# Optimization experiments

Hardware: AMD Instinct MI355X
Metric: run time of the kernel (lower is better)

Reference implementation:

```python
import jax, jax.numpy as jnp
import numpy as np

NEG_INF = -1e38

def wkv(w, u, k, v):
    """Numerically-stable RWKV-4 WKV recurrence.
    w, u: [C] (log-space decay / first-token bonus)
    k, v: [B, T, C]
    returns y: [B, T, C]
    """
    B, T, C = k.shape

    def step(carry, kv):
        p, q, o = carry          # numerator state, denominator state, running log-max; each [B, C]
        kt, vt = kv              # [B, C]
        # output at t (includes the u-boosted current token)
        no = jnp.maximum(o, u + kt)
        A = jnp.exp(o - no)
        Bt = jnp.exp(u + kt - no)
        y = (A * p + Bt * vt) / (A * q + Bt)
        # state update (decay by w, absorb current token)
        no2 = jnp.maximum(w + o, kt)
        A2 = jnp.exp(w + o - no2)
        B2 = jnp.exp(kt - no2)
        return (A2 * p + B2 * vt, A2 * q + B2, no2), y

    init = (jnp.zeros((B, C), k.dtype), jnp.zeros((B, C), k.dtype),
            jnp.full((B, C), NEG_INF, k.dtype))
    kT = jnp.swapaxes(k, 0, 1)   # [T, B, C]
    vT = jnp.swapaxes(v, 0, 1)
    _, ys = jax.lax.scan(step, init, (kT, vT))
    return jnp.swapaxes(ys, 0, 1)


def setup_inputs() -> dict:
    key = jax.random.key(0)
    ks = jax.random.split(key, 10)
    B, T, C = 8, 4096, 512
    scale = 1.0 / np.sqrt(C)
    return {
        "x": jax.random.normal(ks[0], (B, T, C), jnp.float32),
        "spatial_decay": jax.random.normal(ks[1], (C,), jnp.float32),
        "spatial_first": jax.random.normal(ks[2], (C,), jnp.float32),
        "mix_k": jax.random.uniform(ks[3], (1, 1, C), jnp.float32),
        "mix_v": jax.random.uniform(ks[4], (1, 1, C), jnp.float32),
        "mix_r": jax.random.uniform(ks[5], (1, 1, C), jnp.float32),
        "wk": jax.random.normal(ks[6], (C, C), jnp.float32) * scale,
        "wv": jax.random.normal(ks[7], (C, C), jnp.float32) * scale,
        "wr": jax.random.normal(ks[8], (C, C), jnp.float32) * scale,
        "wo": jax.random.normal(ks[9], (C, C), jnp.float32) * scale,
    }


def reference(x, spatial_decay, spatial_first, mix_k, mix_v, mix_r, wk, wv, wr, wo):
    B, T, C = x.shape
    # time_shift: xx[t] = x[t-1], xx[0] = 0  (ZeroPad2d((0,0,1,-1)))
    xx = jnp.pad(x, ((0, 0), (1, 0), (0, 0)))[:, :-1]
    xk = x * mix_k + xx * (1.0 - mix_k)
    xv = x * mix_v + xx * (1.0 - mix_v)
    xr = x * mix_r + xx * (1.0 - mix_r)
    k = jnp.einsum('btc,cd->btd', xk, wk)
    v = jnp.einsum('btc,cd->btd', xv, wv)
    r = jnp.einsum('btc,cd->btd', xr, wr)
    sr = jax.nn.sigmoid(r)
    y = wkv(spatial_decay / T, spatial_first / T, k, v)
    return jnp.einsum('btc,cd->btd', sr * y, wo)
```

## Files before the change

### kernel.cpp

```cpp
#include <hip/hip_runtime.h>

#define BB 8
#define TT 4096
#define CC 512
#define MM (BB * TT)
#define SS 128
#define LL 32

typedef short short8 __attribute__((ext_vector_type(8)));
typedef unsigned short ushort8 __attribute__((ext_vector_type(8)));
typedef float f32x4 __attribute__((ext_vector_type(4)));

__device__ __forceinline__ unsigned short f2bf(float f) {
    unsigned int u = __float_as_uint(f);
    u += 0x7FFFu + ((u >> 16) & 1u);
    return (unsigned short)(u >> 16);
}
__device__ __forceinline__ float bf2f(unsigned short h) {
    return __uint_as_float(((unsigned int)h) << 16);
}

__device__ __forceinline__ void gl_lds16(const void* g, void* l) {
    __builtin_amdgcn_global_load_lds(
        (__attribute__((address_space(1))) void*)(unsigned long long)g,
        (__attribute__((address_space(3))) void*)(unsigned int)(unsigned long long)l,
        16, 0, 0);
}

__device__ __forceinline__ ushort8 pack8(f32x4 a, f32x4 b) {
    ushort8 r;
    r[0] = f2bf(a.x); r[1] = f2bf(a.y); r[2] = f2bf(a.z); r[3] = f2bf(a.w);
    r[4] = f2bf(b.x); r[5] = f2bf(b.y); r[6] = f2bf(b.z); r[7] = f2bf(b.w);
    return r;
}

__global__ __launch_bounds__(256) void prep(
    const float* __restrict__ x,
    const float* __restrict__ mixk, const float* __restrict__ mixv,
    const float* __restrict__ mixr,
    const float* __restrict__ wk, const float* __restrict__ wv,
    const float* __restrict__ wr, const float* __restrict__ wo,
    unsigned short* __restrict__ wT,
    unsigned short* __restrict__ kx, unsigned short* __restrict__ vx,
    unsigned short* __restrict__ rx) {
    __shared__ float t[64][65];
    if (blockIdx.x < 256) {
        const int bid = blockIdx.x;
        const int which = bid >> 6;
        const int rem = bid & 63;
        const int k0 = (rem >> 3) * 64;
        const int n0 = (rem & 7) * 64;
        const float* src = (which == 0) ? wk : (which == 1) ? wv
                         : (which == 2) ? wr : wo;
        const int r = threadIdx.x >> 6;
        const int c = threadIdx.x & 63;
#pragma unroll
        for (int p = 0; p < 16; ++p)
            t[p * 4 + r][c] = src[(size_t)(k0 + p * 4 + r) * CC + n0 + c];
        __syncthreads();
        unsigned short* dst = wT + (size_t)which * (CC * CC);
#pragma unroll
        for (int p = 0; p < 16; ++p)
            dst[(size_t)(n0 + p * 4 + r) * CC + k0 + c] = f2bf(t[c][p * 4 + r]);
        return;
    }
    const int idx = (blockIdx.x - 256) * 256 + threadIdx.x;
    const int row = idx >> 6;
    const int ch  = (idx & 63) * 8;
    const int tt  = row & (TT - 1);
    const size_t off = (size_t)row * CC + ch;
    const float* xr = x + off;

    const f32x4 zero4 = {0.f, 0.f, 0.f, 0.f};
    const f32x4 one4  = {1.f, 1.f, 1.f, 1.f};

    f32x4 xc0 = ((const f32x4*)xr)[0];
    f32x4 xc1 = ((const f32x4*)xr)[1];
    f32x4 xp0 = zero4, xp1 = zero4;
    if (tt != 0) {
        xp0 = ((const f32x4*)(xr - CC))[0];
        xp1 = ((const f32x4*)(xr - CC))[1];
    }

    f32x4 m0, m1;
    m0 = ((const f32x4*)(mixk + ch))[0];
    m1 = ((const f32x4*)(mixk + ch))[1];
    *(ushort8*)(kx + off) = pack8(xc0 * m0 + xp0 * (one4 - m0),
                                  xc1 * m1 + xp1 * (one4 - m1));
    m0 = ((const f32x4*)(mixv + ch))[0];
    m1 = ((const f32x4*)(mixv + ch))[1];
    *(ushort8*)(vx + off) = pack8(xc0 * m0 + xp0 * (one4 - m0),
                                  xc1 * m1 + xp1 * (one4 - m1));
    m0 = ((const f32x4*)(mixr + ch))[0];
    m1 = ((const f32x4*)(mixr + ch))[1];
    *(ushort8*)(rx + off) = pack8(xc0 * m0 + xp0 * (one4 - m0),
                                  xc1 * m1 + xp1 * (one4 - m1));
}

template <bool F32OUT>
__device__ __forceinline__ void gemm_body(
    const unsigned short* __restrict__ A,
    const unsigned short* __restrict__ Bw,
    void* __restrict__ OutP, const int sig,
    const int pm, const int pn) {
    __shared__ unsigned short As[3][128 * 32];
    __shared__ unsigned short Bs[3][256 * 32];

    const int tid = threadIdx.x;
    const int ar = tid >> 2;
    const int cg = (tid & 3) ^ ((tid >> 3) & 3);
    const unsigned short* agA = A  + (size_t)(pm * 128 + ar) * CC + cg * 8;
    const unsigned short* agB = Bw + (size_t)(pn * 256 + ar) * CC + cg * 8;

    const int w = tid >> 6, lane = tid & 63;
    const int wr = w >> 1, wc = w & 1;
    const int q = lane >> 4, l16 = lane & 15;
    const int sw = (q ^ ((l16 >> 1) & 3)) * 8;

    f32x4 acc[4][8];
#pragma unroll
    for (int i = 0; i < 4; i++)
#pragma unroll
        for (int j = 0; j < 8; j++) acc[i][j] = (f32x4){0.f, 0.f, 0.f, 0.f};

#define STG(bi, k0) do {                                                        \
    gl_lds16(agA + (k0), &As[bi][tid * 8]);                                     \
    gl_lds16(agA + (size_t)64 * CC + (k0), &As[bi][(256 + tid) * 8]);           \
    gl_lds16(agB + (k0),                    &Bs[bi][(0 * 256 + tid) * 8]);      \
    gl_lds16(agB + (size_t)64  * CC + (k0), &Bs[bi][(1 * 256 + tid) * 8]);      \
    gl_lds16(agB + (size_t)128 * CC + (k0), &Bs[bi][(2 * 256 + tid) * 8]);      \
    gl_lds16(agB + (size_t)192 * CC + (k0), &Bs[bi][(3 * 256 + tid) * 8]);      \
} while (0)

    STG(0, 0);
    STG(1, 32);

#pragma unroll
    for (int kt = 0; kt < 16; ++kt) {
        const int bi = kt % 3;
        if (kt + 2 < 16) STG((kt + 2) % 3, (kt + 2) * 32);

        if (kt < 14)       asm volatile("s_waitcnt vmcnt(12)" ::: "memory");
        else if (kt == 14) asm volatile("s_waitcnt vmcnt(6)" ::: "memory");
        else               asm volatile("s_waitcnt vmcnt(0)" ::: "memory");
        __builtin_amdgcn_s_barrier();

        __builtin_amdgcn_s_setprio(1);
        short8 a[4], b[8];
#pragma unroll
        for (int i = 0; i < 4; i++)
            a[i] = *(const short8*)&As[bi][(wr * 64 + i * 16 + l16) * 32 + sw];
#pragma unroll
        for (int j = 0; j < 8; j++)
            b[j] = *(const short8*)&Bs[bi][(wc * 128 + j * 16 + l16) * 32 + sw];
#pragma unroll
        for (int i = 0; i < 4; i++)
#pragma unroll
            for (int j = 0; j < 8; j++)
                acc[i][j] = __builtin_amdgcn_mfma_f32_16x16x32_bf16(a[i], b[j], acc[i][j], 0, 0, 0);
        __builtin_amdgcn_s_setprio(0);

        asm volatile("s_waitcnt lgkmcnt(0)" ::: "memory");
        __builtin_amdgcn_s_barrier();
    }
#undef STG

    const size_t rb = (size_t)pm * 128 + wr * 64;
    const int nb = pn * 256 + wc * 128;
    if constexpr (F32OUT) {
        float* Out = (float*)OutP;
#pragma unroll
        for (int i = 0; i < 4; i++)
#pragma unroll
            for (int j = 0; j < 8; j++)
#pragma unroll
                for (int ii = 0; ii < 4; ii++) {
                    const int m = i * 16 + q * 4 + ii;
                    const int n = nb + j * 16 + l16;
                    Out[(rb + m) * CC + n] = acc[i][j][ii];
                }
    } else {
        unsigned short* Out = (unsigned short*)OutP;
#pragma unroll
        for (int i = 0; i < 4; i++)
#pragma unroll
            for (int j = 0; j < 8; j++)
#pragma unroll
                for (int ii = 0; ii < 4; ii++) {
                    const int m = i * 16 + q * 4 + ii;
                    const int n = nb + j * 16 + l16;
                    float val = acc[i][j][ii];
                    if (sig) val = 1.0f / (1.0f + __expf(-val));
                    Out[(rb + m) * CC + n] = f2bf(val);
                }
    }
}

__global__ __launch_bounds__(256, 2) void gemm_kvr3(
    const unsigned short* __restrict__ wT,
    const unsigned short* __restrict__ A0, const unsigned short* __restrict__ A1,
    const unsigned short* __restrict__ A2,
    unsigned short* __restrict__ O0, unsigned short* __restrict__ O1,
    unsigned short* __restrict__ O2) {
    const int z = blockIdx.y;
    const int lin = blockIdx.x;
    const int wg = (lin & 7) * 64 + (lin >> 3);
    const int pm = wg >> 1, pn = wg & 1;
    const unsigned short* A = (z == 0) ? A0 : (z == 1) ? A1 : A2;
    unsigned short* O = (z == 0) ? O0 : (z == 1) ? O1 : O2;
    gemm_body<false>(A, wT + (size_t)z * (CC * CC), O, z == 2, pm, pn);
}

__global__ __launch_bounds__(256, 2) void gemm_out(
    const unsigned short* __restrict__ zb, const unsigned short* __restrict__ woT,
    float* __restrict__ out) {
    const int lin = blockIdx.x;
    const int wg = (lin & 7) * 64 + (lin >> 3);
    gemm_body<true>(zb, woT, out, 0, wg >> 1, wg & 1);
}

__global__ __launch_bounds__(256) void wkv_part1(
    const unsigned short* __restrict__ kb, const unsigned short* __restrict__ vb,
    const float* __restrict__ sd,
    float* __restrict__ sp_, float* __restrict__ sq_, float* __restrict__ so_) {
    const int idx = blockIdx.x * 256 + threadIdx.x;
    const int c = idx & (CC - 1);
    const int b = (idx >> 9) & (BB - 1);
    const int s = idx >> 12;
    const float w = sd[c] * (1.0f / (float)TT);
    const size_t base = ((size_t)b * TT + (size_t)s * LL) * CC + c;
    const unsigned short* kp = kb + base;
    const unsigned short* vp = vb + base;

    float p = 0.f, q = 0.f, o = -1e38f;
#pragma unroll 8
    for (int i = 0; i < LL; ++i) {
        const float kt = bf2f(kp[(size_t)i * CC]);
        const float vt = bf2f(vp[(size_t)i * CC]);
        const float no2 = fmaxf(w + o, kt);
        const float A2  = __expf(w + o - no2);
        const float B2  = __expf(kt - no2);
        p = A2 * p + B2 * vt;
        q = A2 * q + B2;
        o = no2;
    }
    sp_[idx] = p; sq_[idx] = q; so_[idx] = o;
}

__global__ __launch_bounds__(256) void wkv_scan(
    const float* __restrict__ sd,
    float* __restrict__ sp_, float* __restrict__ sq_, float* __restrict__ so_) {
    __shared__ float P[2][128], Q[2][128], O[2][128];
    const int gsub = threadIdx.x >> 7;
    const int s    = threadIdx.x & 127;
    const int g    = blockIdx.x * 2 + gsub;
    const int c    = g & (CC - 1);
    const float wL = sd[c] * ((float)LL / (float)TT);
    const int stride = BB * CC;

    float p = sp_[s * stride + g];
    float q = sq_[s * stride + g];
    float o = so_[s * stride + g];
    P[gsub][s] = p; Q[gsub][s] = q; O[gsub][s] = o;

    float dec = wL;
#pragma unroll
    for (int d = 0; d < 7; ++d) {
        const int off = 1 << d;
        __syncthreads();
        float pl = 0.f, ql = 0.f, ol = -1e38f;
        if (s >= off) {
            pl = P[gsub][s - off]; ql = Q[gsub][s - off]; ol = O[gsub][s - off];
        }
        __syncthreads();
        if (s >= off) {
            const float no = fmaxf(ol + dec, o);
            const float Al = __expf(ol + dec - no);
            const float Bc = __expf(o - no);
            p = Al * pl + Bc * p;
            q = Al * ql + Bc * q;
            o = no;
            P[gsub][s] = p; Q[gsub][s] = q; O[gsub][s] = o;
        }
        dec += dec;
    }
    __syncthreads();
    float ep = 0.f, eq = 0.f, eo = -1e38f;
    if (s > 0) { ep = P[gsub][s - 1]; eq = Q[gsub][s - 1]; eo = O[gsub][s - 1]; }
    sp_[s * stride + g] = ep;
    sq_[s * stride + g] = eq;
    so_[s * stride + g] = eo;
}

__global__ __launch_bounds__(256) void wkv_part3(
    const unsigned short* __restrict__ kb, const unsigned short* __restrict__ vb,
    const unsigned short* __restrict__ srb,
    const float* __restrict__ sd, const float* __restrict__ sf,
    const float* __restrict__ sp_, const float* __restrict__ sq_,
    const float* __restrict__ so_,
    unsigned short* __restrict__ zb) {
    const int idx = blockIdx.x * 256 + threadIdx.x;
    const int c = idx & (CC - 1);
    const int b = (idx >> 9) & (BB - 1);
    const int s = idx >> 12;
    const float w = sd[c] * (1.0f / (float)TT);
    const float u = sf[c] * (1.0f / (float)TT);
    const size_t base = ((size_t)b * TT + (size_t)s * LL) * CC + c;
    const unsigned short* kp = kb + base;
    const unsigned short* vp = vb + base;
    const unsigned short* sp = srb + base;
    unsigned short* zp = zb + base;

    float p = sp_[idx], q = sq_[idx], o = so_[idx];
#pragma unroll 4
    for (int i = 0; i < LL; ++i) {
        const float kt = bf2f(kp[(size_t)i * CC]);
        const float vt = bf2f(vp[(size_t)i * CC]);
        const float sr = bf2f(sp[(size_t)i * CC]);

        const float no = fmaxf(o, u + kt);
        const float A  = __expf(o - no);
        const float Bt = __expf(u + kt - no);
        const float y  = (A * p + Bt * vt) / (A * q + Bt);
        zp[(size_t)i * CC] = f2bf(sr * y);

        const float no2 = fmaxf(w + o, kt);
        const float A2  = __expf(w + o - no2);
        const float B2  = __expf(kt - no2);
        p = A2 * p + B2 * vt;
        q = A2 * q + B2;
        o = no2;
    }
}

extern "C" void kernel_launch(void* const* d_in, const int* in_sizes, int n_in,
                              void* d_out, int out_size, void* d_ws, size_t ws_size,
                              hipStream_t stream) {
    const float* x  = (const float*)d_in[0];
    const float* sd = (const float*)d_in[1];
    const float* sf = (const float*)d_in[2];
    const float* mk = (const float*)d_in[3];
    const float* mv = (const float*)d_in[4];
    const float* mr = (const float*)d_in[5];
    const float* wk = (const float*)d_in[6];
    const float* wv = (const float*)d_in[7];
    const float* wr = (const float*)d_in[8];
    const float* wo = (const float*)d_in[9];
    float* out = (float*)d_out;

    char* ws = (char*)d_ws;
    unsigned short* wT = (unsigned short*)ws;
    unsigned short* b1 = wT + (size_t)4 * CC * CC;
    unsigned short* b2 = b1 + (size_t)MM * CC;
    unsigned short* b3 = b2 + (size_t)MM * CC;
    unsigned short* b4 = b3 + (size_t)MM * CC;
    unsigned short* b5 = b4 + (size_t)MM * CC;
    float* sp_ = (float*)(b5 + (size_t)MM * CC);
    float* sq_ = sp_ + (size_t)SS * BB * CC;
    float* so_ = sq_ + (size_t)SS * BB * CC;
    unsigned short* woT = wT + (size_t)3 * CC * CC;
    unsigned short* srS = (unsigned short*)d_out;

    prep<<<dim3(256 + (MM * CC / 8) / 256), 256, 0, stream>>>(
        x, mk, mv, mr, wk, wv, wr, wo, wT, b1, b2, b3);

    gemm_kvr3<<<dim3(512, 3), 256, 0, stream>>>(wT, b1, b2, b3, b4, b5, srS);

    wkv_part1<<<dim3((SS * BB * CC) / 256), 256, 0, stream>>>(b4, b5, sd, sp_, sq_, so_);
    wkv_scan<<<dim3((BB * CC) / 2), 256, 0, stream>>>(sd, sp_, sq_, so_);
    wkv_part3<<<dim3((SS * BB * CC) / 256), 256, 0, stream>>>(
        b4, b5, srS, sd, sf, sp_, sq_, so_, b1);

    gemm_out<<<dim3(512), 256, 0, stream>>>(b1, woT, out);
}
```

Measured before the change: 297.7 us.

## Switch GEMMs to 256x256 tiles with 8 waves and double-buffered K=64 stages

Replaces the 128x256 tile GEMM (4 waves, triple-buffered K=32 stages) with a 256x256 tile run by 512 threads (8 waves in a 2x4 layout). It double-buffers K=64 stages and interleaves global-to-LDS loads in quarter-steps between MFMA groups. The kvr3 launch flattens to 768 one-dimensional blocks with an XCD-aware remap that also selects z. The goal is more operand reuse per LDS byte and fewer blocks, at the cost of more LDS per block, more barriers per K step, and only 256 blocks for the output GEMM, which may underfill the GPU.

```diff
diff --git a/kernel.cpp b/kernel.cpp
--- a/kernel.cpp
+++ b/kernel.cpp
@@ -98,81 +98,114 @@
 }
 
 template <bool F32OUT>
-__device__ __forceinline__ void gemm_body(
+__device__ __forceinline__ void gemm256_body(
     const unsigned short* __restrict__ A,
     const unsigned short* __restrict__ Bw,
     void* __restrict__ OutP, const int sig,
     const int pm, const int pn) {
-    __shared__ unsigned short As[3][128 * 32];
-    __shared__ unsigned short Bs[3][256 * 32];
+    __shared__ unsigned short As[32768];
+    __shared__ unsigned short Bs[32768];
 
     const int tid = threadIdx.x;
-    const int ar = tid >> 2;
     const int cg = (tid & 3) ^ ((tid >> 3) & 3);
-    const unsigned short* agA = A  + (size_t)(pm * 128 + ar) * CC + cg * 8;
-    const unsigned short* agB = Bw + (size_t)(pn * 256 + ar) * CC + cg * 8;
-
-    const int w = tid >> 6, lane = tid & 63;
-    const int wr = w >> 1, wc = w & 1;
+    const unsigned short* agA = A  + (size_t)(pm * 256 + (tid >> 2)) * CC + cg * 8;
+    const unsigned short* agB = Bw + (size_t)(pn * 256 + (tid >> 2)) * CC + cg * 8;
+
+    const int wid = tid >> 6, lane = tid & 63;
+    const int wr = wid >> 2, wc = wid & 3;
     const int q = lane >> 4, l16 = lane & 15;
-    const int sw = (q ^ ((l16 >> 1) & 3)) * 8;
-
-    f32x4 acc[4][8];
-#pragma unroll
-    for (int i = 0; i < 4; i++)
-#pragma unroll
-        for (int j = 0; j < 8; j++) acc[i][j] = (f32x4){0.f, 0.f, 0.f, 0.f};
-
-#define STG(bi, k0) do {                                                        \
-    gl_lds16(agA + (k0), &As[bi][tid * 8]);                                     \
-    gl_lds16(agA + (size_t)64 * CC + (k0), &As[bi][(256 + tid) * 8]);           \
-    gl_lds16(agB + (k0),                    &Bs[bi][(0 * 256 + tid) * 8]);      \
-    gl_lds16(agB + (size_t)64  * CC + (k0), &Bs[bi][(1 * 256 + tid) * 8]);      \
-    gl_lds16(agB + (size_t)128 * CC + (k0), &Bs[bi][(2 * 256 + tid) * 8]);      \
-    gl_lds16(agB + (size_t)192 * CC + (k0), &Bs[bi][(3 * 256 + tid) * 8]);      \
+    const int swz = (q ^ ((l16 >> 1) & 3)) * 8;
+
+    const int aro = (wr * 128 + l16) * 32 + swz;
+    const int bro = (wc * 64 + l16) * 32 + swz;
+
+    f32x4 acc[8][4];
+#pragma unroll
+    for (int i = 0; i < 8; i++)
+#pragma unroll
+        for (int j = 0; j < 4; j++) acc[i][j] = (f32x4){0.f, 0.f, 0.f, 0.f};
+
+#define STG_A(sl_, h_, kt_) do {                                               \
+    gl_lds16(agA + ((kt_) * 64 + (h_) * 32),                                   \
+             &As[(sl_) * 16384 + (h_) * 8192 + tid * 8]);                      \
+    gl_lds16(agA + (size_t)128 * CC + ((kt_) * 64 + (h_) * 32),                \
+             &As[(sl_) * 16384 + (h_) * 8192 + 4096 + tid * 8]);               \
 } while (0)
-
-    STG(0, 0);
-    STG(1, 32);
-
-#pragma unroll
-    for (int kt = 0; kt < 16; ++kt) {
-        const int bi = kt % 3;
-        if (kt + 2 < 16) STG((kt + 2) % 3, (kt + 2) * 32);
-
-        if (kt < 14)       asm volatile("s_waitcnt vmcnt(12)" ::: "memory");
-        else if (kt == 14) asm volatile("s_waitcnt vmcnt(6)" ::: "memory");
-        else               asm volatile("s_waitcnt vmcnt(0)" ::: "memory");
-        __builtin_amdgcn_s_barrier();
-
-        __builtin_amdgcn_s_setprio(1);
-        short8 a[4], b[8];
-#pragma unroll
-        for (int i = 0; i < 4; i++)
-            a[i] = *(const short8*)&As[bi][(wr * 64 + i * 16 + l16) * 32 + sw];
-#pragma unroll
-        for (int j = 0; j < 8; j++)
-            b[j] = *(const short8*)&Bs[bi][(wc * 128 + j * 16 + l16) * 32 + sw];
-#pragma unroll
-        for (int i = 0; i < 4; i++)
-#pragma unroll
-            for (int j = 0; j < 8; j++)
-                acc[i][j] = __builtin_amdgcn_mfma_f32_16x16x32_bf16(a[i], b[j], acc[i][j], 0, 0, 0);
-        __builtin_amdgcn_s_setprio(0);
-
+#define STG_B(sl_, h_, kt_) do {                                               \
+    gl_lds16(agB + ((kt_) * 64 + (h_) * 32),                                   \
+             &Bs[(sl_) * 16384 + (h_) * 8192 + tid * 8]);                      \
+    gl_lds16(agB + (size_t)128 * CC + ((kt_) * 64 + (h_) * 32),                \
+             &Bs[(sl_) * 16384 + (h_) * 8192 + 4096 + tid * 8]);               \
+} while (0)
+
+    STG_A(0, 0, 0); STG_B(0, 0, 0); STG_A(0, 1, 0); STG_B(0, 1, 0);
+    asm volatile("s_waitcnt vmcnt(4)" ::: "memory");
+    __builtin_amdgcn_s_barrier();
+
+    short8 a[4], b[4];
+
+#define MFMA16(IB)                                                             \
+    __builtin_amdgcn_s_setprio(1);                                             \
+    _Pragma("unroll")                                                          \
+    for (int i = 0; i < 4; ++i)                                                \
+        _Pragma("unroll")                                                      \
+        for (int j = 0; j < 4; ++j)                                            \
+            acc[(IB) + i][j] = __builtin_amdgcn_mfma_f32_16x16x32_bf16(        \
+                a[i], b[j], acc[(IB) + i][j], 0, 0, 0);                        \
+    __builtin_amdgcn_s_setprio(0);
+
+#pragma unroll
+    for (int t = 0; t < 8; ++t) {
+        const int sl = t & 1, ns = sl ^ 1;
+        const int ab = sl * 16384;
+        if (t < 7) STG_A(ns, 0, t + 1);
+#pragma unroll
+        for (int j = 0; j < 4; ++j) b[j] = *(const short8*)&Bs[ab + bro + j * 512];
+#pragma unroll
+        for (int i = 0; i < 4; ++i) a[i] = *(const short8*)&As[ab + aro + i * 512];
+        __builtin_amdgcn_s_barrier();
         asm volatile("s_waitcnt lgkmcnt(0)" ::: "memory");
-        __builtin_amdgcn_s_barrier();
-    }
-#undef STG
-
-    const size_t rb = (size_t)pm * 128 + wr * 64;
-    const int nb = pn * 256 + wc * 128;
+        MFMA16(0)
+        __builtin_amdgcn_s_barrier();
+        if (t < 7) STG_B(ns, 0, t + 1);
+#pragma unroll
+        for (int i = 0; i < 4; ++i) a[i] = *(const short8*)&As[ab + aro + 2048 + i * 512];
+        if (t < 7) asm volatile("s_waitcnt vmcnt(4)" ::: "memory");
+        else       asm volatile("s_waitcnt vmcnt(0)" ::: "memory");
+        __builtin_amdgcn_s_barrier();
+        asm volatile("s_waitcnt lgkmcnt(0)" ::: "memory");
+        MFMA16(4)
+        __builtin_amdgcn_s_barrier();
+        if (t < 7) STG_A(ns, 1, t + 1);
+#pragma unroll
+        for (int j = 0; j < 4; ++j) b[j] = *(const short8*)&Bs[ab + 8192 + bro + j * 512];
+#pragma unroll
+        for (int i = 0; i < 4; ++i) a[i] = *(const short8*)&As[ab + 8192 + aro + i * 512];
+        __builtin_amdgcn_s_barrier();
+        asm volatile("s_waitcnt lgkmcnt(0)" ::: "memory");
+        MFMA16(0)
+        __builtin_amdgcn_s_barrier();
+        if (t < 7) STG_B(ns, 1, t + 1);
+#pragma unroll
+        for (int i = 0; i < 4; ++i) a[i] = *(const short8*)&As[ab + 8192 + aro + 2048 + i * 512];
+        if (t < 7) asm volatile("s_waitcnt vmcnt(4)" ::: "memory");
+        __builtin_amdgcn_s_barrier();
+        asm volatile("s_waitcnt lgkmcnt(0)" ::: "memory");
+        MFMA16(4)
+        __builtin_amdgcn_s_barrier();
+    }
+#undef MFMA16
+#undef STG_A
+#undef STG_B
+
+    const size_t rb = (size_t)pm * 256 + wr * 128;
+    const int nb = pn * 256 + wc * 64;
     if constexpr (F32OUT) {
         float* Out = (float*)OutP;
 #pragma unroll
-        for (int i = 0; i < 4; i++)
-#pragma unroll
-            for (int j = 0; j < 8; j++)
+        for (int i = 0; i < 8; i++)
+#pragma unroll
+            for (int j = 0; j < 4; j++)
 #pragma unroll
                 for (int ii = 0; ii < 4; ii++) {
                     const int m = i * 16 + q * 4 + ii;
@@ -182,9 +215,9 @@
     } else {
         unsigned short* Out = (unsigned short*)OutP;
 #pragma unroll
-        for (int i = 0; i < 4; i++)
-#pragma unroll
-            for (int j = 0; j < 8; j++)
+        for (int i = 0; i < 8; i++)
+#pragma unroll
+            for (int j = 0; j < 4; j++)
 #pragma unroll
                 for (int ii = 0; ii < 4; ii++) {
                     const int m = i * 16 + q * 4 + ii;
@@ -196,27 +229,28 @@
     }
 }
 
-__global__ __launch_bounds__(256, 2) void gemm_kvr3(
+__global__ __launch_bounds__(512, 2) void gemm_kvr3(
     const unsigned short* __restrict__ wT,
     const unsigned short* __restrict__ A0, const unsigned short* __restrict__ A1,
     const unsigned short* __restrict__ A2,
     unsigned short* __restrict__ O0, unsigned short* __restrict__ O1,
     unsigned short* __restrict__ O2) {
-    const int z = blockIdx.y;
     const int lin = blockIdx.x;
-    const int wg = (lin & 7) * 64 + (lin >> 3);
-    const int pm = wg >> 1, pn = wg & 1;
+    const int wg = (lin & 7) * 96 + (lin >> 3);
+    const int z = wg >> 8;
+    const int r = wg & 255;
+    const int pm = r >> 1, pn = r & 1;
     const unsigned short* A = (z == 0) ? A0 : (z == 1) ? A1 : A2;
     unsigned short* O = (z == 0) ? O0 : (z == 1) ? O1 : O2;
-    gemm_body<false>(A, wT + (size_t)z * (CC * CC), O, z == 2, pm, pn);
-}
-
-__global__ __launch_bounds__(256, 2) void gemm_out(
+    gemm256_body<false>(A, wT + (size_t)z * (CC * CC), O, z == 2, pm, pn);
+}
+
+__global__ __launch_bounds__(512, 2) void gemm_out(
     const unsigned short* __restrict__ zb, const unsigned short* __restrict__ woT,
     float* __restrict__ out) {
     const int lin = blockIdx.x;
-    const int wg = (lin & 7) * 64 + (lin >> 3);
-    gemm_body<true>(zb, woT, out, 0, wg >> 1, wg & 1);
+    const int wg = (lin & 7) * 32 + (lin >> 3);
+    gemm256_body<true>(zb, woT, out, 0, wg >> 1, wg & 1);
 }
 
 __global__ __launch_bounds__(256) void wkv_part1(
@@ -364,12 +398,12 @@
     prep<<<dim3(256 + (MM * CC / 8) / 256), 256, 0, stream>>>(
         x, mk, mv, mr, wk, wv, wr, wo, wT, b1, b2, b3);
 
-    gemm_kvr3<<<dim3(512, 3), 256, 0, stream>>>(wT, b1, b2, b3, b4, b5, srS);
+    gemm_kvr3<<<dim3(768), 512, 0, stream>>>(wT, b1, b2, b3, b4, b5, srS);
 
     wkv_part1<<<dim3((SS * BB * CC) / 256), 256, 0, stream>>>(b4, b5, sd, sp_, sq_, so_);
     wkv_scan<<<dim3((BB * CC) / 2), 256, 0, stream>>>(sd, sp_, sq_, so_);
     wkv_part3<<<dim3((SS * BB * CC) / 256), 256, 0, stream>>>(
         b4, b5, srS, sd, sf, sp_, sq_, so_, b1);
 
-    gemm_out<<<dim3(512), 256, 0, stream>>>(b1, woT, out);
-}
+    gemm_out<<<dim3(256), 512, 0, stream>>>(b1, woT, out);
+}
```

Result: slower. 311.5 us (+4.6%).

## Fuse time-shift token mixing into KVR GEMM A-operand load

Applied to the files above, without the earlier changes.

The separate prep pass that wrote bf16 mixed k/v/r inputs is removed. The KVR GEMM now reads fp32 x and its shifted row directly, applies the mix, converts to bf16 and stores into LDS, with double buffering (down from triple) and software pipelining of the register loads. Weight transpose becomes its own small kernel. This cuts about three full activation-sized writes and reads, but each GEMM block reloads x once per z, and the A-path now goes through registers instead of direct global-to-LDS loads.

```diff
diff --git a/kernel.cpp b/kernel.cpp
--- a/kernel.cpp
+++ b/kernel.cpp
@@ -34,83 +34,188 @@
     return r;
 }
 
-__global__ __launch_bounds__(256) void prep(
+__global__ __launch_bounds__(256) void transpose_w(
+    const float* __restrict__ wk, const float* __restrict__ wv,
+    const float* __restrict__ wr, const float* __restrict__ wo,
+    unsigned short* __restrict__ wT) {
+    __shared__ float t[64][65];
+    const int which = blockIdx.z;
+    const float* src = (which == 0) ? wk : (which == 1) ? wv : (which == 2) ? wr : wo;
+    const int k0 = blockIdx.y * 64;
+    const int n0 = blockIdx.x * 64;
+    const int r = threadIdx.x >> 6;
+    const int c = threadIdx.x & 63;
+#pragma unroll
+    for (int p = 0; p < 16; ++p)
+        t[p * 4 + r][c] = src[(size_t)(k0 + p * 4 + r) * CC + n0 + c];
+    __syncthreads();
+    unsigned short* dst = wT + (size_t)which * (CC * CC);
+#pragma unroll
+    for (int p = 0; p < 16; ++p)
+        dst[(size_t)(n0 + p * 4 + r) * CC + k0 + c] = f2bf(t[c][p * 4 + r]);
+}
+
+__global__ __launch_bounds__(256, 2) void gemm_kvr3(
+    const unsigned short* __restrict__ wT,
     const float* __restrict__ x,
     const float* __restrict__ mixk, const float* __restrict__ mixv,
     const float* __restrict__ mixr,
-    const float* __restrict__ wk, const float* __restrict__ wv,
-    const float* __restrict__ wr, const float* __restrict__ wo,
-    unsigned short* __restrict__ wT,
-    unsigned short* __restrict__ kx, unsigned short* __restrict__ vx,
-    unsigned short* __restrict__ rx) {
-    __shared__ float t[64][65];
-    if (blockIdx.x < 256) {
-        const int bid = blockIdx.x;
-        const int which = bid >> 6;
-        const int rem = bid & 63;
-        const int k0 = (rem >> 3) * 64;
-        const int n0 = (rem & 7) * 64;
-        const float* src = (which == 0) ? wk : (which == 1) ? wv
-                         : (which == 2) ? wr : wo;
-        const int r = threadIdx.x >> 6;
-        const int c = threadIdx.x & 63;
-#pragma unroll
-        for (int p = 0; p < 16; ++p)
-            t[p * 4 + r][c] = src[(size_t)(k0 + p * 4 + r) * CC + n0 + c];
-        __syncthreads();
-        unsigned short* dst = wT + (size_t)which * (CC * CC);
-#pragma unroll
-        for (int p = 0; p < 16; ++p)
-            dst[(size_t)(n0 + p * 4 + r) * CC + k0 + c] = f2bf(t[c][p * 4 + r]);
-        return;
-    }
-    const int idx = (blockIdx.x - 256) * 256 + threadIdx.x;
-    const int row = idx >> 6;
-    const int ch  = (idx & 63) * 8;
-    const int tt  = row & (TT - 1);
-    const size_t off = (size_t)row * CC + ch;
-    const float* xr = x + off;
-
-    const f32x4 zero4 = {0.f, 0.f, 0.f, 0.f};
-    const f32x4 one4  = {1.f, 1.f, 1.f, 1.f};
-
-    f32x4 xc0 = ((const f32x4*)xr)[0];
-    f32x4 xc1 = ((const f32x4*)xr)[1];
-    f32x4 xp0 = zero4, xp1 = zero4;
-    if (tt != 0) {
-        xp0 = ((const f32x4*)(xr - CC))[0];
-        xp1 = ((const f32x4*)(xr - CC))[1];
-    }
-
-    f32x4 m0, m1;
-    m0 = ((const f32x4*)(mixk + ch))[0];
-    m1 = ((const f32x4*)(mixk + ch))[1];
-    *(ushort8*)(kx + off) = pack8(xc0 * m0 + xp0 * (one4 - m0),
-                                  xc1 * m1 + xp1 * (one4 - m1));
-    m0 = ((const f32x4*)(mixv + ch))[0];
-    m1 = ((const f32x4*)(mixv + ch))[1];
-    *(ushort8*)(vx + off) = pack8(xc0 * m0 + xp0 * (one4 - m0),
-                                  xc1 * m1 + xp1 * (one4 - m1));
-    m0 = ((const f32x4*)(mixr + ch))[0];
-    m1 = ((const f32x4*)(mixr + ch))[1];
-    *(ushort8*)(rx + off) = pack8(xc0 * m0 + xp0 * (one4 - m0),
-                                  xc1 * m1 + xp1 * (one4 - m1));
-}
-
-template <bool F32OUT>
-__device__ __forceinline__ void gemm_body(
-    const unsigned short* __restrict__ A,
-    const unsigned short* __restrict__ Bw,
-    void* __restrict__ OutP, const int sig,
-    const int pm, const int pn) {
-    __shared__ unsigned short As[3][128 * 32];
-    __shared__ unsigned short Bs[3][256 * 32];
+    unsigned short* __restrict__ O0, unsigned short* __restrict__ O1,
+    unsigned short* __restrict__ O2) {
+    __shared__ unsigned short As[2][128 * 32];
+    __shared__ unsigned short Bs[2][256 * 32];
+
+    const int z = blockIdx.y;
+    const int lin = blockIdx.x;
+    const int wg = (lin & 7) * 64 + (lin >> 3);
+    const int pm = wg >> 1, pn = wg & 1;
+    const float* mixp = (z == 0) ? mixk : (z == 1) ? mixv : mixr;
+    unsigned short* O = (z == 0) ? O0 : (z == 1) ? O1 : O2;
+    const unsigned short* Bw = wT + (size_t)z * (CC * CC);
 
     const int tid = threadIdx.x;
     const int ar = tid >> 2;
     const int cg = (tid & 3) ^ ((tid >> 3) & 3);
-    const unsigned short* agA = A  + (size_t)(pm * 128 + ar) * CC + cg * 8;
+    const int row0 = pm * 128 + ar;
+    const int t0 = (row0 & (TT - 1)) == 0;
+    const float gate = t0 ? 0.f : 1.f;
+    const float* xr0 = x + (size_t)row0 * CC + cg * 8;
+    const float* xq0 = x + (size_t)(t0 ? row0 : row0 - 1) * CC + cg * 8;
+    const float* xr1 = xr0 + (size_t)64 * CC;
+    const float* xq1 = xr1 - CC;
+    const float* mp  = mixp + cg * 8;
     const unsigned short* agB = Bw + (size_t)(pn * 256 + ar) * CC + cg * 8;
+
+    const int w = tid >> 6, lane = tid & 63;
+    const int wr = w >> 1, wc = w & 1;
+    const int q = lane >> 4, l16 = lane & 15;
+    const int sw = (q ^ ((l16 >> 1) & 3)) * 8;
+
+    f32x4 acc[4][8];
+#pragma unroll
+    for (int i = 0; i < 4; i++)
+#pragma unroll
+        for (int j = 0; j < 8; j++) acc[i][j] = (f32x4){0.f, 0.f, 0.f, 0.f};
+
+#define STG_B(bi, k0) do {                                                      \
+    gl_lds16(agB + (k0),                    &Bs[bi][(0 * 256 + tid) * 8]);      \
+    gl_lds16(agB + (size_t)64  * CC + (k0), &Bs[bi][(1 * 256 + tid) * 8]);      \
+    gl_lds16(agB + (size_t)128 * CC + (k0), &Bs[bi][(2 * 256 + tid) * 8]);      \
+    gl_lds16(agB + (size_t)192 * CC + (k0), &Bs[bi][(3 * 256 + tid) * 8]);      \
+} while (0)
+
+#define MIXW(bi)                                                                \
+    do {                                                                        \
+        f32x4 g0 = p00 * gate, g1 = p01 * gate;                                 \
+        f32x4 r00 = g0 + m0 * (c00 - g0);                                       \
+        f32x4 r01 = g1 + m1 * (c01 - g1);                                       \
+        f32x4 r10 = p10 + m0 * (c10 - p10);                                     \
+        f32x4 r11 = p11 + m1 * (c11 - p11);                                     \
+        *(ushort8*)&As[bi][tid * 8]         = pack8(r00, r01);                  \
+        *(ushort8*)&As[bi][(256 + tid) * 8] = pack8(r10, r11);                  \
+    } while (0)
+
+#define ALOAD(kc)                                                               \
+    f32x4 c00 = *(const f32x4*)(xr0 + (kc));                                    \
+    f32x4 c01 = *(const f32x4*)(xr0 + (kc) + 4);                                \
+    f32x4 p00 = *(const f32x4*)(xq0 + (kc));                                    \
+    f32x4 p01 = *(const f32x4*)(xq0 + (kc) + 4);                                \
+    f32x4 c10 = *(const f32x4*)(xr1 + (kc));                                    \
+    f32x4 c11 = *(const f32x4*)(xr1 + (kc) + 4);                                \
+    f32x4 p10 = *(const f32x4*)(xq1 + (kc));                                    \
+    f32x4 p11 = *(const f32x4*)(xq1 + (kc) + 4);                                \
+    f32x4 m0  = *(const f32x4*)(mp + (kc));                                     \
+    f32x4 m1  = *(const f32x4*)(mp + (kc) + 4);
+
+    {
+        ALOAD(0);
+        STG_B(0, 0);
+        MIXW(0);
+        asm volatile("s_waitcnt vmcnt(0)" ::: "memory");
+        asm volatile("s_waitcnt lgkmcnt(0)" ::: "memory");
+        __builtin_amdgcn_s_barrier();
+    }
+
+#pragma unroll
+    for (int kt = 0; kt < 16; ++kt) {
+        const int cur = kt & 1, nb = cur ^ 1;
+        if (kt < 15) {
+            ALOAD((kt + 1) * 32);
+            STG_B(nb, (kt + 1) * 32);
+            asm volatile("s_waitcnt vmcnt(14)" ::: "memory");
+            __builtin_amdgcn_s_barrier();
+
+            __builtin_amdgcn_s_setprio(1);
+            short8 a[4], b[8];
+#pragma unroll
+            for (int i = 0; i < 4; i++)
+                a[i] = *(const short8*)&As[cur][(wr * 64 + i * 16 + l16) * 32 + sw];
+#pragma unroll
+            for (int j = 0; j < 8; j++)
+                b[j] = *(const short8*)&Bs[cur][(wc * 128 + j * 16 + l16) * 32 + sw];
+#pragma unroll
+            for (int i = 0; i < 4; i++)
+#pragma unroll
+                for (int j = 0; j < 8; j++)
+                    acc[i][j] = __builtin_amdgcn_mfma_f32_16x16x32_bf16(a[i], b[j], acc[i][j], 0, 0, 0);
+            __builtin_amdgcn_s_setprio(0);
+
+            MIXW(nb);
+            asm volatile("s_waitcnt lgkmcnt(0)" ::: "memory");
+            __builtin_amdgcn_s_barrier();
+        } else {
+            asm volatile("s_waitcnt vmcnt(0)" ::: "memory");
+            __builtin_amdgcn_s_barrier();
+            short8 a[4], b[8];
+#pragma unroll
+            for (int i = 0; i < 4; i++)
+                a[i] = *(const short8*)&As[cur][(wr * 64 + i * 16 + l16) * 32 + sw];
+#pragma unroll
+            for (int j = 0; j < 8; j++)
+                b[j] = *(const short8*)&Bs[cur][(wc * 128 + j * 16 + l16) * 32 + sw];
+#pragma unroll
+            for (int i = 0; i < 4; i++)
+#pragma unroll
+                for (int j = 0; j < 8; j++)
+                    acc[i][j] = __builtin_amdgcn_mfma_f32_16x16x32_bf16(a[i], b[j], acc[i][j], 0, 0, 0);
+        }
+    }
+#undef ALOAD
+#undef MIXW
+#undef STG_B
+
+    const bool sig = (z == 2);
+    const size_t rb = (size_t)pm * 128 + wr * 64;
+    const int nb2 = pn * 256 + wc * 128;
+#pragma unroll
+    for (int i = 0; i < 4; i++)
+#pragma unroll
+        for (int j = 0; j < 8; j++)
+#pragma unroll
+            for (int ii = 0; ii < 4; ii++) {
+                const int m = i * 16 + q * 4 + ii;
+                const int n = nb2 + j * 16 + l16;
+                float val = acc[i][j][ii];
+                if (sig) val = 1.0f / (1.0f + __expf(-val));
+                O[(rb + m) * CC + n] = f2bf(val);
+            }
+}
+
+__global__ __launch_bounds__(256, 2) void gemm_out(
+    const unsigned short* __restrict__ zb, const unsigned short* __restrict__ woT,
+    float* __restrict__ out) {
+    __shared__ unsigned short As[3][128 * 32];
+    __shared__ unsigned short Bs[3][256 * 32];
+
+    const int lin = blockIdx.x;
+    const int wg = (lin & 7) * 64 + (lin >> 3);
+    const int pm = wg >> 1, pn = wg & 1;
+
+    const int tid = threadIdx.x;
+    const int ar = tid >> 2;
+    const int cg = (tid & 3) ^ ((tid >> 3) & 3);
+    const unsigned short* agA = zb  + (size_t)(pm * 128 + ar) * CC + cg * 8;
+    const unsigned short* agB = woT + (size_t)(pn * 256 + ar) * CC + cg * 8;
 
     const int w = tid >> 6, lane = tid & 63;
     const int wr = w >> 1, wc = w & 1;
@@ -167,56 +272,16 @@
 
     const size_t rb = (size_t)pm * 128 + wr * 64;
     const int nb = pn * 256 + wc * 128;
-    if constexpr (F32OUT) {
-        float* Out = (float*)OutP;
-#pragma unroll
-        for (int i = 0; i < 4; i++)
-#pragma unroll
-            for (int j = 0; j < 8; j++)
-#pragma unroll
-                for (int ii = 0; ii < 4; ii++) {
-                    const int m = i * 16 + q * 4 + ii;
-                    const int n = nb + j * 16 + l16;
-                    Out[(rb + m) * CC + n] = acc[i][j][ii];
-                }
-    } else {
-        unsigned short* Out = (unsigned short*)OutP;
-#pragma unroll
-        for (int i = 0; i < 4; i++)
-#pragma unroll
-            for (int j = 0; j < 8; j++)
-#pragma unroll
-                for (int ii = 0; ii < 4; ii++) {
-                    const int m = i * 16 + q * 4 + ii;
-                    const int n = nb + j * 16 + l16;
-                    float val = acc[i][j][ii];
-                    if (sig) val = 1.0f / (1.0f + __expf(-val));
-                    Out[(rb + m) * CC + n] = f2bf(val);
-                }
-    }
-}
-
-__global__ __launch_bounds__(256, 2) void gemm_kvr3(
-    const unsigned short* __restrict__ wT,
-    const unsigned short* __restrict__ A0, const unsigned short* __restrict__ A1,
-    const unsigned short* __restrict__ A2,
-    unsigned short* __restrict__ O0, unsigned short* __restrict__ O1,
-    unsigned short* __restrict__ O2) {
-    const int z = blockIdx.y;
-    const int lin = blockIdx.x;
-    const int wg = (lin & 7) * 64 + (lin >> 3);
-    const int pm = wg >> 1, pn = wg & 1;
-    const unsigned short* A = (z == 0) ? A0 : (z == 1) ? A1 : A2;
-    unsigned short* O = (z == 0) ? O0 : (z == 1) ? O1 : O2;
-    gemm_body<false>(A, wT + (size_t)z * (CC * CC), O, z == 2, pm, pn);
-}
-
-__global__ __launch_bounds__(256, 2) void gemm_out(
-    const unsigned short* __restrict__ zb, const unsigned short* __restrict__ woT,
-    float* __restrict__ out) {
-    const int lin = blockIdx.x;
-    const int wg = (lin & 7) * 64 + (lin >> 3);
-    gemm_body<true>(zb, woT, out, 0, wg >> 1, wg & 1);
+#pragma unroll
+    for (int i = 0; i < 4; i++)
+#pragma unroll
+        for (int j = 0; j < 8; j++)
+#pragma unroll
+            for (int ii = 0; ii < 4; ii++) {
+                const int m = i * 16 + q * 4 + ii;
+                const int n = nb + j * 16 + l16;
+                out[(rb + m) * CC + n] = acc[i][j][ii];
+            }
 }
 
 __global__ __launch_bounds__(256) void wkv_part1(
@@ -350,26 +415,23 @@
 
     char* ws = (char*)d_ws;
     unsigned short* wT = (unsigned short*)ws;
-    unsigned short* b1 = wT + (size_t)4 * CC * CC;
-    unsigned short* b2 = b1 + (size_t)MM * CC;
-    unsigned short* b3 = b2 + (size_t)MM * CC;
-    unsigned short* b4 = b3 + (size_t)MM * CC;
-    unsigned short* b5 = b4 + (size_t)MM * CC;
-    float* sp_ = (float*)(b5 + (size_t)MM * CC);
+    unsigned short* bk = wT + (size_t)4 * CC * CC;
+    unsigned short* bv = bk + (size_t)MM * CC;
+    unsigned short* bz = bv + (size_t)MM * CC;
+    float* sp_ = (float*)(bz + (size_t)MM * CC);
     float* sq_ = sp_ + (size_t)SS * BB * CC;
     float* so_ = sq_ + (size_t)SS * BB * CC;
     unsigned short* woT = wT + (size_t)3 * CC * CC;
     unsigned short* srS = (unsigned short*)d_out;
 
-    prep<<<dim3(256 + (MM * CC / 8) / 256), 256, 0, stream>>>(
-        x, mk, mv, mr, wk, wv, wr, wo, wT, b1, b2, b3);
-
-    gemm_kvr3<<<dim3(512, 3), 256, 0, stream>>>(wT, b1, b2, b3, b4, b5, srS);
-
-    wkv_part1<<<dim3((SS * BB * CC) / 256), 256, 0, stream>>>(b4, b5, sd, sp_, sq_, so_);
+    transpose_w<<<dim3(8, 8, 4), 256, 0, stream>>>(wk, wv, wr, wo, wT);
+
+    gemm_kvr3<<<dim3(512, 3), 256, 0, stream>>>(wT, x, mk, mv, mr, bk, bv, srS);
+
+    wkv_part1<<<dim3((SS * BB * CC) / 256), 256, 0, stream>>>(bk, bv, sd, sp_, sq_, so_);
     wkv_scan<<<dim3((BB * CC) / 2), 256, 0, stream>>>(sd, sp_, sq_, so_);
     wkv_part3<<<dim3((SS * BB * CC) / 256), 256, 0, stream>>>(
-        b4, b5, srS, sd, sf, sp_, sq_, so_, b1);
-
-    gemm_out<<<dim3(512), 256, 0, stream>>>(b1, woT, out);
-}
+        bk, bv, srS, sd, sf, sp_, sq_, so_, bz);
+
+    gemm_out<<<dim3(512), 256, 0, stream>>>(bz, woT, out);
+}
```

Result: no change. 301.2 us (+1.2%).
